# Optimization experiments

Hardware: AMD Instinct MI355X
Metric: run time of the kernel (lower is better)

Reference implementation:

```python
import jax, jax.numpy as jnp
import numpy as np

B, DX, DY, H = 512, 128, 128, 512


def setup_inputs() -> dict:
    key = jax.random.key(0)
    ks = jax.random.split(key, 5)
    x = jax.random.normal(ks[0], (B, DX), dtype=jnp.float32)
    y = jax.random.normal(ks[1], (B, DY), dtype=jnp.float32)
    # torch nn.Linear-style weights [out_features, in_features], small init scale
    W1 = jax.random.normal(ks[2], (H, DX + DY), dtype=jnp.float32) * 0.05
    b1 = jnp.zeros((H,), dtype=jnp.float32)
    W2 = jax.random.normal(ks[3], (H, H), dtype=jnp.float32) * 0.05
    b2 = jnp.zeros((H,), dtype=jnp.float32)
    W3 = jax.random.normal(ks[4], (1, H), dtype=jnp.float32) * 0.05
    b3 = jnp.zeros((1,), dtype=jnp.float32)
    return {"x": x, "y": y, "W1": W1, "b1": b1, "W2": W2, "b2": b2, "W3": W3, "b3": b3}


def reference(x, y, W1, b1, W2, b2, W3, b3):
    # Original: pair (row i, col j) of the *returned* (transposed) matrix is
    # f(concat(x[i], y[j])). We fuse the B^2 concat + first Linear into two
    # B x H matmuls broadcast-summed (mathematically identical).
    dimX = x.shape[1]
    hx = jnp.einsum("id,hd->ih", x, W1[:, :dimX])          # [B, H]
    hy = jnp.einsum("jd,hd->jh", y, W1[:, dimX:])          # [B, H]
    h = jax.nn.relu(hx[:, None, :] + hy[None, :, :] + b1)   # [B, B, H]
    h = jax.nn.relu(jnp.einsum("ijh,kh->ijk", h, W2) + b2)  # [B, B, H]
    out = jnp.einsum("ijh,h->ij", h, W3[0]) + b3[0]         # [B, B]
    return out
```

## Files before the change

kernel.cpp:

```cpp
#include <hip/hip_runtime.h>
#include <hip/hip_bf16.h>

#define Bn  512
#define DXn 128
#define Hn  512

using bf16x8 = __attribute__((ext_vector_type(8))) short;
using f32x4  = __attribute__((ext_vector_type(4))) float;

static __device__ __forceinline__ unsigned int pkbf(float lo, float hi) {
    union { __hip_bfloat162 b; unsigned int u; } cv;
    cv.b = __float22bfloat162_rn(make_float2(lo, hi));
    return cv.u;
}

static __device__ __forceinline__ void gld_lds16(const void* g, void* l) {
    __builtin_amdgcn_global_load_lds(
        (const __attribute__((address_space(1))) unsigned int*)g,
        (__attribute__((address_space(3))) unsigned int*)l,
        16, 0, 0);
}

__global__ __launch_bounds__(256) void prep_fused(
    const float* __restrict__ x, const float* __restrict__ y,
    const float* __restrict__ W1, const float* __restrict__ b1,
    const float* __restrict__ W2,
    float* __restrict__ hxb, float* __restrict__ hyv,
    unsigned short* __restrict__ w2s)
{
    const int bid = blockIdx.x;
    const int t = threadIdx.x;

    if (bid >= 256) {
        const int T = (bid - 256) * 256 + t;
        const int l = T & 63;
        const int c = (T >> 6) & 31;
        const int s = T >> 11;
        const int row = c * 16 + (l & 15);
        const int col = s * 32 + (l >> 4) * 8;
        const float* p = &W2[row * Hn + col];
        const float4 v0 = *(const float4*)p;
        const float4 v1 = *(const float4*)(p + 4);
        uint4 pk;
        pk.x = pkbf(v0.x, v0.y);
        pk.y = pkbf(v0.z, v0.w);
        pk.z = pkbf(v1.x, v1.y);
        pk.w = pkbf(v1.z, v1.w);
        *(uint4*)(w2s + (size_t)T * 8) = pk;
        return;
    }

    const int which = bid >> 7;
    const int rem = bid & 127;
    const int i0 = (rem >> 3) * 32;
    const int h0 = (rem & 7) * 64;
    const float* __restrict__ src = which ? y : x;
    float* __restrict__ dst = which ? hyv : hxb;
    const int off = which ? DXn : 0;

    __shared__ float xs[32][132];
    __shared__ float ws[64][132];
    #pragma unroll
    for (int it = 0; it < 4; ++it) {
        const int fi = it * 256 + t;
        const int r = fi >> 5, q = fi & 31;
        *(float4*)&xs[r][q * 4] = *(const float4*)&src[(i0 + r) * DXn + q * 4];
    }
    #pragma unroll
    for (int it = 0; it < 8; ++it) {
        const int fi = it * 256 + t;
        const int r = fi >> 5, q = fi & 31;
        *(float4*)&ws[r][q * 4] = *(const float4*)&W1[(h0 + r) * (2 * DXn) + off + q * 4];
    }
    __syncthreads();

    const int tx = t & 15;
    const int ty = t >> 4;
    float acc[2][4];
    #pragma unroll
    for (int v = 0; v < 2; ++v)
        #pragma unroll
        for (int u = 0; u < 4; ++u)
            acc[v][u] = which ? 0.0f : b1[h0 + tx + u * 16];

    #pragma unroll 4
    for (int c4 = 0; c4 < 32; ++c4) {
        const float4 xv0 = *(const float4*)&xs[ty * 2 + 0][c4 * 4];
        const float4 xv1 = *(const float4*)&xs[ty * 2 + 1][c4 * 4];
        #pragma unroll
        for (int u = 0; u < 4; ++u) {
            const float4 wv = *(const float4*)&ws[tx + u * 16][c4 * 4];
            acc[0][u] = fmaf(xv0.x, wv.x, fmaf(xv0.y, wv.y, fmaf(xv0.z, wv.z, fmaf(xv0.w, wv.w, acc[0][u]))));
            acc[1][u] = fmaf(xv1.x, wv.x, fmaf(xv1.y, wv.y, fmaf(xv1.z, wv.z, fmaf(xv1.w, wv.w, acc[1][u]))));
        }
    }
    #pragma unroll
    for (int v = 0; v < 2; ++v)
        #pragma unroll
        for (int u = 0; u < 4; ++u)
            dst[(size_t)(i0 + ty * 2 + v) * Hn + h0 + tx + u * 16] = acc[v][u];
}

static __device__ __forceinline__ void gen_a_half(
    unsigned short* a_us, const float* __restrict__ hyrow,
    const float* __restrict__ hxrow, int p, int w, int l, int lg)
{
    #pragma unroll
    for (int q = 0; q < 8; ++q) {
        const int h0 = (p * 8 + q) * 32 + lg * 8;
        const float4 a0 = *(const float4*)(hyrow + h0);
        const float4 a1 = *(const float4*)(hyrow + h0 + 4);
        const float4 x0 = *(const float4*)(hxrow + h0);
        const float4 x1 = *(const float4*)(hxrow + h0 + 4);
        uint4 pk;
        pk.x = pkbf(fmaxf(a0.x + x0.x, 0.f), fmaxf(a0.y + x0.y, 0.f));
        pk.y = pkbf(fmaxf(a0.z + x0.z, 0.f), fmaxf(a0.w + x0.w, 0.f));
        pk.z = pkbf(fmaxf(a1.x + x1.x, 0.f), fmaxf(a1.y + x1.y, 0.f));
        pk.w = pkbf(fmaxf(a1.z + x1.z, 0.f), fmaxf(a1.w + x1.w, 0.f));
        *(uint4*)(a_us + ((size_t)(w * 8 + q) * 64 + l) * 8) = pk;
    }
}

__global__ __launch_bounds__(512, 2) void critic_main(
    const float* __restrict__ hxb, const float* __restrict__ hyv,
    const unsigned short* __restrict__ w2s, const float* __restrict__ b2,
    const float* __restrict__ W3, const float* __restrict__ b3,
    float* __restrict__ out)
{
    __shared__ __align__(16) unsigned char smem[131072];
    unsigned short* a_us = (unsigned short*)smem;
    unsigned char* b_base = smem + 65536;
    float* red = (float*)smem;

    const int i   = blockIdx.y;
    const int j0  = blockIdx.x * 128;
    const int tid = threadIdx.x;
    const int w   = tid >> 6;
    const int l   = tid & 63;
    const int lg  = l >> 4;
    const int lm  = l & 15;

    const float* __restrict__ hxrow = &hxb[(size_t)i * Hn];
    const int r = w * 16 + lm;
    const float* __restrict__ hyrow = &hyv[(size_t)(j0 + r) * Hn];
    const unsigned char* __restrict__ w2b = (const unsigned char*)w2s;

    #pragma unroll
    for (int n = 0; n < 4; ++n) {
        const int c = w * 4 + n;
        gld_lds16(w2b + (size_t)c * 1024 + l * 16, b_base + c * 1024);
    }
    gen_a_half(a_us, hyrow, hxrow, 0, w, l, lg);
    __syncthreads();

    f32x4 acc[8][4] = {};

    #pragma unroll
    for (int p = 0; p < 2; ++p) {
        if (p == 1) {
            gen_a_half(a_us, hyrow, hxrow, 1, w, l, lg);
            __syncthreads();
        }
        #pragma unroll
        for (int q = 0; q < 8; ++q) {
            const int s = p * 8 + q;
            if (s < 15) {
                const int sn = s + 1;
                const int nb = sn & 1;
                #pragma unroll
                for (int n = 0; n < 4; ++n) {
                    const int c = w * 4 + n;
                    gld_lds16(w2b + (size_t)sn * 32768 + c * 1024 + l * 16,
                              b_base + nb * 32768 + c * 1024);
                }
            }
            const int cb = s & 1;
            bf16x8 a[8], b[4];
            #pragma unroll
            for (int fj = 0; fj < 4; ++fj)
                b[fj] = *(const bf16x8*)(b_base + cb * 32768 + (w * 4 + fj) * 1024 + l * 16);
            #pragma unroll
            for (int fi = 0; fi < 8; ++fi)
                a[fi] = *(const bf16x8*)(a_us + ((size_t)(fi * 8 + q) * 64 + l) * 8);
            __builtin_amdgcn_s_setprio(1);
            #pragma unroll
            for (int fi = 0; fi < 8; ++fi)
                #pragma unroll
                for (int fj = 0; fj < 4; ++fj)
                    acc[fi][fj] = __builtin_amdgcn_mfma_f32_16x16x32_bf16(
                        a[fi], b[fj], acc[fi][fj], 0, 0, 0);
            __builtin_amdgcn_s_setprio(0);
            __syncthreads();
        }
    }

    float b2v[4], w3v[4];
    #pragma unroll
    for (int fj = 0; fj < 4; ++fj) {
        const int k = w * 64 + fj * 16 + lm;
        b2v[fj] = b2[k];
        w3v[fj] = W3[k];
    }
    float rp[8][4];
    #pragma unroll
    for (int fi = 0; fi < 8; ++fi) {
        #pragma unroll
        for (int qq = 0; qq < 4; ++qq) {
            float ssum = 0.f;
            #pragma unroll
            for (int fj = 0; fj < 4; ++fj) {
                float c = acc[fi][fj][qq] + b2v[fj];
                c = fmaxf(c, 0.f);
                ssum = fmaf(c, w3v[fj], ssum);
            }
            rp[fi][qq] = ssum;
        }
    }
    #pragma unroll
    for (int m = 1; m < 16; m <<= 1) {
        #pragma unroll
        for (int fi = 0; fi < 8; ++fi)
            #pragma unroll
            for (int qq = 0; qq < 4; ++qq)
                rp[fi][qq] += __shfl_xor(rp[fi][qq], m, 64);
    }

    if (lm == 0) {
        #pragma unroll
        for (int fi = 0; fi < 8; ++fi)
            #pragma unroll
            for (int qq = 0; qq < 4; ++qq)
                red[w * 128 + fi * 16 + lg * 4 + qq] = rp[fi][qq];
    }
    __syncthreads();
    if (tid < 128) {
        float ssum = 0.f;
        #pragma unroll
        for (int ww = 0; ww < 8; ++ww) ssum += red[ww * 128 + tid];
        out[(size_t)i * Bn + j0 + tid] = ssum + b3[0];
    }
}

extern "C" void kernel_launch(void* const* d_in, const int* in_sizes, int n_in,
                              void* d_out, int out_size, void* d_ws, size_t ws_size,
                              hipStream_t stream) {
    const float* x  = (const float*)d_in[0];
    const float* y  = (const float*)d_in[1];
    const float* W1 = (const float*)d_in[2];
    const float* b1 = (const float*)d_in[3];
    const float* W2 = (const float*)d_in[4];
    const float* b2 = (const float*)d_in[5];
    const float* W3 = (const float*)d_in[6];
    const float* b3 = (const float*)d_in[7];
    float* out = (float*)d_out;

    char* ws = (char*)d_ws;
    float* hxb = (float*)ws;
    float* hyv = (float*)(ws + (size_t)Bn * Hn * 4);
    unsigned short* w2s = (unsigned short*)(ws + (size_t)2 * Bn * Hn * 4);

    prep_fused<<<dim3(384), dim3(256), 0, stream>>>(x, y, W1, b1, W2, hxb, hyv, w2s);
    critic_main<<<dim3(Bn / 128, Bn), dim3(512), 0, stream>>>(hxb, hyv, w2s, b2, W3, b3, out);
}
```

Before: 263.2 us.

## Double-buffer A tile per k-step and interleave generation with MFMA halves

Replaces the two-phase generation of the full 64KB A tile with a per-k-step 8KB double-buffered A tile, generated one step ahead while MFMAs run. Each iteration splits the MFMA work into two halves separated by barriers, with the next A slice computed between them, and uses manual vmcnt/lgkmcnt waits and raw s_barrier instead of __syncthreads. Shared memory drops from 128KB to 80KB. The aim is to hide the A-generation and global-load latency behind matrix work. In exchange it adds more barriers per step, and the hand-placed waitcnts risk hazards if the counts are wrong.

```diff
diff --git a/kernel.cpp b/kernel.cpp
--- a/kernel.cpp
+++ b/kernel.cpp
@@ -7,6 +7,8 @@
 
 using bf16x8 = __attribute__((ext_vector_type(8))) short;
 using f32x4  = __attribute__((ext_vector_type(4))) float;
+
+#define VMCNT(n) asm volatile("s_waitcnt vmcnt(" #n ")" ::: "memory")
 
 static __device__ __forceinline__ unsigned int pkbf(float lo, float hi) {
     union { __hip_bfloat162 b; unsigned int u; } cv;
@@ -101,35 +103,13 @@
             dst[(size_t)(i0 + ty * 2 + v) * Hn + h0 + tx + u * 16] = acc[v][u];
 }
 
-static __device__ __forceinline__ void gen_a_half(
-    unsigned short* a_us, const float* __restrict__ hyrow,
-    const float* __restrict__ hxrow, int p, int w, int l, int lg)
-{
-    #pragma unroll
-    for (int q = 0; q < 8; ++q) {
-        const int h0 = (p * 8 + q) * 32 + lg * 8;
-        const float4 a0 = *(const float4*)(hyrow + h0);
-        const float4 a1 = *(const float4*)(hyrow + h0 + 4);
-        const float4 x0 = *(const float4*)(hxrow + h0);
-        const float4 x1 = *(const float4*)(hxrow + h0 + 4);
-        uint4 pk;
-        pk.x = pkbf(fmaxf(a0.x + x0.x, 0.f), fmaxf(a0.y + x0.y, 0.f));
-        pk.y = pkbf(fmaxf(a0.z + x0.z, 0.f), fmaxf(a0.w + x0.w, 0.f));
-        pk.z = pkbf(fmaxf(a1.x + x1.x, 0.f), fmaxf(a1.y + x1.y, 0.f));
-        pk.w = pkbf(fmaxf(a1.z + x1.z, 0.f), fmaxf(a1.w + x1.w, 0.f));
-        *(uint4*)(a_us + ((size_t)(w * 8 + q) * 64 + l) * 8) = pk;
-    }
-}
-
 __global__ __launch_bounds__(512, 2) void critic_main(
     const float* __restrict__ hxb, const float* __restrict__ hyv,
     const unsigned short* __restrict__ w2s, const float* __restrict__ b2,
     const float* __restrict__ W3, const float* __restrict__ b3,
     float* __restrict__ out)
 {
-    __shared__ __align__(16) unsigned char smem[131072];
-    unsigned short* a_us = (unsigned short*)smem;
-    unsigned char* b_base = smem + 65536;
+    __shared__ __align__(16) unsigned char smem[81920];
     float* red = (float*)smem;
 
     const int i   = blockIdx.y;
@@ -141,57 +121,100 @@
     const int lm  = l & 15;
 
     const float* __restrict__ hxrow = &hxb[(size_t)i * Hn];
-    const int r = w * 16 + lm;
-    const float* __restrict__ hyrow = &hyv[(size_t)(j0 + r) * Hn];
+    const float* __restrict__ hyrow = &hyv[(size_t)(j0 + w * 16 + lm) * Hn];
     const unsigned char* __restrict__ w2b = (const unsigned char*)w2s;
 
-    #pragma unroll
-    for (int n = 0; n < 4; ++n) {
-        const int c = w * 4 + n;
-        gld_lds16(w2b + (size_t)c * 1024 + l * 16, b_base + c * 1024);
-    }
-    gen_a_half(a_us, hyrow, hxrow, 0, w, l, lg);
-    __syncthreads();
+    {
+        const int hb = lg * 8;
+        const float4 sy0 = *(const float4*)(hyrow + hb);
+        const float4 sy1 = *(const float4*)(hyrow + hb + 4);
+        const float4 sx0 = *(const float4*)(hxrow + hb);
+        const float4 sx1 = *(const float4*)(hxrow + hb + 4);
+        #pragma unroll
+        for (int n = 0; n < 4; ++n) {
+            const int c = w * 4 + n;
+            gld_lds16(w2b + (size_t)c * 1024 + l * 16,
+                      smem + 16384 + c * 1024);
+        }
+        uint4 pk;
+        pk.x = pkbf(fmaxf(sy0.x + sx0.x, 0.f), fmaxf(sy0.y + sx0.y, 0.f));
+        pk.y = pkbf(fmaxf(sy0.z + sx0.z, 0.f), fmaxf(sy0.w + sx0.w, 0.f));
+        pk.z = pkbf(fmaxf(sy1.x + sx1.x, 0.f), fmaxf(sy1.y + sx1.y, 0.f));
+        pk.w = pkbf(fmaxf(sy1.z + sx1.z, 0.f), fmaxf(sy1.w + sx1.w, 0.f));
+        *(uint4*)(smem + (w * 64 + l) * 16) = pk;
+        asm volatile("s_waitcnt lgkmcnt(0)" ::: "memory");
+        __builtin_amdgcn_sched_barrier(0);
+        __builtin_amdgcn_s_barrier();
+    }
 
     f32x4 acc[8][4] = {};
 
     #pragma unroll
-    for (int p = 0; p < 2; ++p) {
-        if (p == 1) {
-            gen_a_half(a_us, hyrow, hxrow, 1, w, l, lg);
-            __syncthreads();
-        }
-        #pragma unroll
-        for (int q = 0; q < 8; ++q) {
-            const int s = p * 8 + q;
-            if (s < 15) {
-                const int sn = s + 1;
-                const int nb = sn & 1;
-                #pragma unroll
-                for (int n = 0; n < 4; ++n) {
-                    const int c = w * 4 + n;
-                    gld_lds16(w2b + (size_t)sn * 32768 + c * 1024 + l * 16,
-                              b_base + nb * 32768 + c * 1024);
-                }
+    for (int t = 0; t < 16; ++t) {
+        const int ct = t & 1;
+        const unsigned short* ab = (const unsigned short*)(smem + ct * 8192);
+        const unsigned char*  bb = smem + 16384 + ct * 32768;
+        unsigned short* abn = (unsigned short*)(smem + (ct ^ 1) * 8192);
+        unsigned char*  bbn = smem + 16384 + (ct ^ 1) * 32768;
+
+        float4 sy0, sy1, sx0, sx1;
+        if (t < 15) {
+            const int hb = (t + 1) * 32 + lg * 8;
+            sy0 = *(const float4*)(hyrow + hb);
+            sy1 = *(const float4*)(hyrow + hb + 4);
+            sx0 = *(const float4*)(hxrow + hb);
+            sx1 = *(const float4*)(hxrow + hb + 4);
+            #pragma unroll
+            for (int n = 0; n < 4; ++n) {
+                const int c = w * 4 + n;
+                gld_lds16(w2b + (size_t)(t + 1) * 32768 + c * 1024 + l * 16,
+                          bbn + c * 1024);
             }
-            const int cb = s & 1;
-            bf16x8 a[8], b[4];
+        }
+        if (t < 15) { VMCNT(8); } else { VMCNT(0); }
+
+        bf16x8 b[4], a0[4];
+        #pragma unroll
+        for (int fj = 0; fj < 4; ++fj)
+            b[fj] = *(const bf16x8*)(bb + (w * 4 + fj) * 1024 + l * 16);
+        #pragma unroll
+        for (int fi = 0; fi < 4; ++fi)
+            a0[fi] = *(const bf16x8*)(ab + ((size_t)fi * 64 + l) * 8);
+
+        __builtin_amdgcn_s_barrier();
+        __builtin_amdgcn_s_setprio(1);
+        #pragma unroll
+        for (int fi = 0; fi < 4; ++fi)
             #pragma unroll
             for (int fj = 0; fj < 4; ++fj)
-                b[fj] = *(const bf16x8*)(b_base + cb * 32768 + (w * 4 + fj) * 1024 + l * 16);
-            #pragma unroll
-            for (int fi = 0; fi < 8; ++fi)
-                a[fi] = *(const bf16x8*)(a_us + ((size_t)(fi * 8 + q) * 64 + l) * 8);
-            __builtin_amdgcn_s_setprio(1);
-            #pragma unroll
-            for (int fi = 0; fi < 8; ++fi)
-                #pragma unroll
-                for (int fj = 0; fj < 4; ++fj)
-                    acc[fi][fj] = __builtin_amdgcn_mfma_f32_16x16x32_bf16(
-                        a[fi], b[fj], acc[fi][fj], 0, 0, 0);
-            __builtin_amdgcn_s_setprio(0);
-            __syncthreads();
-        }
+                acc[fi][fj] = __builtin_amdgcn_mfma_f32_16x16x32_bf16(
+                    a0[fi], b[fj], acc[fi][fj], 0, 0, 0);
+        __builtin_amdgcn_s_setprio(0);
+        __builtin_amdgcn_s_barrier();
+
+        bf16x8 a1[4];
+        #pragma unroll
+        for (int fi = 0; fi < 4; ++fi)
+            a1[fi] = *(const bf16x8*)(ab + ((size_t)(fi + 4) * 64 + l) * 8);
+        if (t < 15) {
+            uint4 pk;
+            pk.x = pkbf(fmaxf(sy0.x + sx0.x, 0.f), fmaxf(sy0.y + sx0.y, 0.f));
+            pk.y = pkbf(fmaxf(sy0.z + sx0.z, 0.f), fmaxf(sy0.w + sx0.w, 0.f));
+            pk.z = pkbf(fmaxf(sy1.x + sx1.x, 0.f), fmaxf(sy1.y + sx1.y, 0.f));
+            pk.w = pkbf(fmaxf(sy1.z + sx1.z, 0.f), fmaxf(sy1.w + sx1.w, 0.f));
+            *(uint4*)((unsigned char*)abn + (w * 64 + l) * 16) = pk;
+        }
+        __builtin_amdgcn_s_setprio(1);
+        #pragma unroll
+        for (int fi = 0; fi < 4; ++fi)
+            #pragma unroll
+            for (int fj = 0; fj < 4; ++fj)
+                acc[fi + 4][fj] = __builtin_amdgcn_mfma_f32_16x16x32_bf16(
+                    a1[fi], b[fj], acc[fi + 4][fj], 0, 0, 0);
+        __builtin_amdgcn_s_setprio(0);
+        asm volatile("s_waitcnt lgkmcnt(0)" ::: "memory");
+        __builtin_amdgcn_sched_barrier(0);
+        __builtin_amdgcn_s_barrier();
     }
 
     float b2v[4], w3v[4];
@@ -225,6 +248,7 @@
                 rp[fi][qq] += __shfl_xor(rp[fi][qq], m, 64);
     }
 
+    __syncthreads();
     if (lm == 0) {
         #pragma unroll
         for (int fi = 0; fi < 8; ++fi)
```

Result: slower. 273.9 us (+4.1%).
